# Optimization experiments

Hardware: AMD Instinct MI355X
Metric: run time of the kernel (lower is better)

## Reference

```python
import jax, jax.numpy as jnp
import numpy as np

N_NODES = 50000
N_EDGES = 800000
D_MODEL = 256
NUM_HEADS = 8
HEAD_DIM = D_MODEL // NUM_HEADS
D_FF = 2 * D_MODEL
NEG_SLOPE = 0.2
BN_EPS = 1e-5


def setup_inputs() -> dict:
    key = jax.random.key(0)
    ks = jax.random.split(key, 16)
    x = jax.random.normal(ks[0], (N_NODES, D_MODEL), dtype=jnp.float32)
    # edges guaranteed self-loop-free (remove_self_loops is then a no-op)
    src = jax.random.randint(ks[1], (N_EDGES,), 0, N_NODES)
    off = jax.random.randint(ks[2], (N_EDGES,), 1, N_NODES)
    dst = (src + off) % N_NODES
    edge_index = jnp.stack([src, dst]).astype(jnp.int64)

    def lin(k, fi, fo):
        s = 1.0 / np.sqrt(fi)
        return jax.random.uniform(k, (fi, fo), jnp.float32, -s, s)

    inp = {
        'x': x, 'edge_index': edge_index,
        'Wq': lin(ks[3], D_MODEL, D_MODEL), 'bq': jnp.zeros((D_MODEL,), jnp.float32),
        'Wk': lin(ks[4], D_MODEL, D_MODEL), 'bk': jnp.zeros((D_MODEL,), jnp.float32),
        'Wv': lin(ks[5], D_MODEL, D_MODEL), 'bv': jnp.zeros((D_MODEL,), jnp.float32),
        'Wo': lin(ks[6], D_MODEL, D_MODEL), 'bo': jnp.zeros((D_MODEL,), jnp.float32),
        'W1': lin(ks[7], D_MODEL, D_FF), 'b1': jnp.zeros((D_FF,), jnp.float32),
        'W2': lin(ks[8], D_FF, D_MODEL), 'b2': jnp.zeros((D_MODEL,), jnp.float32),
        'bn1_g': jnp.ones((D_MODEL,), jnp.float32), 'bn1_b': jnp.zeros((D_MODEL,), jnp.float32),
        'bn2_g': jnp.ones((D_MODEL,), jnp.float32), 'bn2_b': jnp.zeros((D_MODEL,), jnp.float32),
    }
    return inp


def _batch_norm(h, g, b):
    mean = jnp.mean(h, axis=0)
    var = jnp.mean((h - mean) ** 2, axis=0)  # biased var, torch BN training mode
    return (h - mean) * jax.lax.rsqrt(var + BN_EPS) * g + b


def reference(x, edge_index, Wq, bq, Wk, bk, Wv, bv, Wo, bo, W1, b1, W2, b2,
              bn1_g, bn1_b, bn2_g, bn2_b):
    N = x.shape[0]
    Qh = (x @ Wq + bq).reshape(N, NUM_HEADS, HEAD_DIM)
    Kh = (x @ Wk + bk).reshape(N, NUM_HEADS, HEAD_DIM)
    Vh = (x @ Wv + bv).reshape(N, NUM_HEADS, HEAD_DIM)
    # per-node score q_n . k_n / sqrt(C)  -> [N, H]
    s = jnp.einsum('nhc,nhc->nh', Qh, Kh) / jnp.sqrt(jnp.float32(HEAD_DIM))

    # add self loops (input edges contain no self loops)
    loops = jnp.arange(N, dtype=edge_index.dtype)
    src = jnp.concatenate([edge_index[0], loops])
    dst = jnp.concatenate([edge_index[1], loops])

    alpha = jax.nn.leaky_relu(s[src] + s[dst], NEG_SLOPE)  # [Etot, H]
    # segment softmax over destination neighborhoods
    m = jax.ops.segment_max(alpha, dst, num_segments=N)
    e = jnp.exp(alpha - m[dst])
    denom = jax.ops.segment_sum(e, dst, num_segments=N)
    a = e / denom[dst]

    msg = Vh[src] * a[:, :, None]                     # [Etot, H, C]
    attn = jax.ops.segment_sum(msg, dst, num_segments=N).reshape(N, D_MODEL)

    h = attn @ Wo + bo
    h = x + h
    h = _batch_norm(h, bn1_g, bn1_b)
    h2 = jax.nn.relu(h @ W1 + b1) @ W2 + b2
    h = _batch_norm(h + h2, bn2_g, bn2_b)
    return h
```

## Files before the change

### kernel.cpp

```cpp
#include <hip/hip_runtime.h>
#include <hip/hip_bf16.h>

#define NN 50000
#define MP 50048
#define DM 256
#define NH 8
#define HD 32
#define DFF 512

typedef unsigned short u16;
typedef unsigned char u8;
typedef __attribute__((ext_vector_type(8))) short bf16x8;
typedef __attribute__((ext_vector_type(4))) short bf16x4;
typedef __attribute__((ext_vector_type(4))) float f32x4;

__device__ __forceinline__ float leaky(float a) { return a > 0.f ? a : 0.2f * a; }

__device__ __forceinline__ float b2f(u16 s) {
    union { float f; unsigned u; } v; v.u = ((unsigned)s) << 16; return v.f;
}
__device__ __forceinline__ u16 f2b(float f) {
    union { float f; unsigned u; } v; v.f = f;
    unsigned r = v.u + 0x7FFFu + ((v.u >> 16) & 1u);
    return (u16)(r >> 16);
}

__device__ __forceinline__ void f8enc8(const float* v, unsigned* w2) {
#if __has_builtin(__builtin_amdgcn_cvt_pk_fp8_f32)
    int lo = 0, hi = 0;
    lo = __builtin_amdgcn_cvt_pk_fp8_f32(v[0], v[1], lo, false);
    lo = __builtin_amdgcn_cvt_pk_fp8_f32(v[2], v[3], lo, true);
    hi = __builtin_amdgcn_cvt_pk_fp8_f32(v[4], v[5], hi, false);
    hi = __builtin_amdgcn_cvt_pk_fp8_f32(v[6], v[7], hi, true);
    w2[0] = (unsigned)lo; w2[1] = (unsigned)hi;
#else
    unsigned r[8];
#pragma unroll
    for (int j = 0; j < 8; ++j) {
        union { float f; unsigned u; } x; x.f = v[j];
        const unsigned s = (x.u >> 24) & 0x80u;
        float a = fabsf(v[j]);
        if (a > 448.f) a = 448.f;
        if (a < 0.0009765625f) { r[j] = s; continue; }
        if (a < 0.015625f) {
            int m = (int)(a * 512.f + 0.5f); if (m > 7) m = 7;
            r[j] = s | (unsigned)m; continue;
        }
        union { float f; unsigned u; } w; w.f = a;
        unsigned rr = w.u + 0x7FFFFu + ((w.u >> 20) & 1u);
        int e2 = (int)((rr >> 23) & 0xffu) - 127;
        unsigned m3 = (rr >> 20) & 7u;
        if (e2 > 8) { e2 = 8; m3 = 7u; }
        r[j] = s | ((unsigned)(e2 + 7) << 3) | m3;
    }
    w2[0] = r[0] | (r[1] << 8) | (r[2] << 16) | (r[3] << 24);
    w2[1] = r[4] | (r[5] << 8) | (r[6] << 16) | (r[7] << 24);
#endif
}

__device__ __forceinline__ void f8dec8(uint2 uv, float* f) {
#if __has_builtin(__builtin_amdgcn_cvt_pk_f32_fp8)
    auto p0 = __builtin_amdgcn_cvt_pk_f32_fp8((int)uv.x, false);
    auto p1 = __builtin_amdgcn_cvt_pk_f32_fp8((int)uv.x, true);
    auto p2 = __builtin_amdgcn_cvt_pk_f32_fp8((int)uv.y, false);
    auto p3 = __builtin_amdgcn_cvt_pk_f32_fp8((int)uv.y, true);
    f[0] = p0[0]; f[1] = p0[1]; f[2] = p1[0]; f[3] = p1[1];
    f[4] = p2[0]; f[5] = p2[1]; f[6] = p3[0]; f[7] = p3[1];
#else
#pragma unroll
    for (int j = 0; j < 8; ++j) {
        const unsigned b = (j < 4 ? uv.x >> (8 * j) : uv.y >> (8 * (j - 4))) & 0xffu;
        const unsigned s = (b & 0x80u) << 24;
        const unsigned em = b & 0x7fu;
        union { unsigned u; float f; } n; n.u = s | ((em + 0x3C0u) << 20);
        float dn = (float)(int)(em & 7u) * 0.001953125f;
        dn = (b & 0x80u) ? -dn : dn;
        f[j] = (em >= 8u) ? n.f : dn;
    }
#endif
}

#define ASYNC16(gp, lp) __builtin_amdgcn_global_load_lds( \
    (const __attribute__((address_space(1))) void*)(gp),  \
    (__attribute__((address_space(3))) void*)(lp), 16, 0, 0)

template<int RELU, int RES, int K, int MODE>
__global__ __launch_bounds__(256, 4) void gemm_bf16(
    const u16* __restrict__ A, const u16* __restrict__ Bt,
    const float* __restrict__ bias, const void* __restrict__ res,
    const float* __restrict__ ra, const float* __restrict__ rb,
    u16* __restrict__ C, u8* __restrict__ Cv, float* __restrict__ gsums,
    int M, int N)
{
    union SMu {
        struct { u16 As[128][64]; u16 Bs[128][64]; } t;
        struct { u16 eps[128][136]; float lsum[128], lsq[128]; } e;
    };
    __shared__ __align__(16) SMu sm;

    const int tid = threadIdx.x;
    const int wave = tid >> 6, lane = tid & 63;

    const int gx = gridDim.x;
    const int nwg = gx * gridDim.y;
    const int orig = blockIdx.y * gx + blockIdx.x;
    const int q = nwg >> 3, r = nwg & 7;
    const int xcd = orig & 7, rank = orig >> 3;
    const int wg = (xcd < r ? xcd * (q + 1) : r * (q + 1) + (xcd - r) * q) + rank;
    const int m0 = (wg / gx) * 128, n0 = (wg % gx) * 128;

    const int wr = (wave >> 1) * 64, wc = (wave & 1) * 64;

    f32x4 acc[4][4] = {};

    const int srow = wave * 32 + (lane >> 3);
    const int scol = ((lane & 7) * 8) ^ (((lane >> 3) & 7) << 3);
    const int rx = (lane & 7) << 4;

#pragma unroll
    for (int k0 = 0; k0 < K; k0 += 64) {
#pragma unroll
        for (int i = 0; i < 4; ++i)
            ASYNC16(A + (size_t)(m0 + srow + i * 8) * K + k0 + scol,
                    &sm.t.As[wave * 32 + i * 8][0]);
#pragma unroll
        for (int i = 0; i < 4; ++i)
            ASYNC16(Bt + (size_t)(n0 + srow + i * 8) * K + k0 + scol,
                    &sm.t.Bs[wave * 32 + i * 8][0]);
        __syncthreads();
        const char* asb = (const char*)&sm.t.As[0][0];
        const char* bsb = (const char*)&sm.t.Bs[0][0];
#pragma unroll
        for (int kk = 0; kk < 64; kk += 32) {
            const int kb = (kk + (lane >> 4) * 8) * 2;
            bf16x8 av[4], bv[4];
#pragma unroll
            for (int m = 0; m < 4; ++m) {
                const int rr_ = wr + m * 16 + (lane & 15);
                av[m] = *(const bf16x8*)(asb + rr_ * 128 + (kb ^ rx));
            }
#pragma unroll
            for (int n = 0; n < 4; ++n) {
                const int rr_ = wc + n * 16 + (lane & 15);
                bv[n] = *(const bf16x8*)(bsb + rr_ * 128 + (kb ^ rx));
            }
#pragma unroll
            for (int m = 0; m < 4; ++m)
#pragma unroll
                for (int n = 0; n < 4; ++n)
                    acc[m][n] = __builtin_amdgcn_mfma_f32_16x16x32_bf16(
                        av[m], bv[n], acc[m][n], 0, 0, 0);
        }
        __syncthreads();
    }

    const int col_l = lane & 15, rgrp = (lane >> 4) * 4;
#pragma unroll
    for (int m = 0; m < 4; ++m)
#pragma unroll
        for (int rr2 = 0; rr2 < 4; ++rr2) {
            const int lr = wr + m * 16 + rgrp + rr2;
#pragma unroll
            for (int n = 0; n < 4; ++n)
                sm.e.eps[lr][wc + n * 16 + col_l] = f2b(acc[m][n][rr2]);
        }
    __syncthreads();
    if (MODE == 2) {
        if (tid < 128) { sm.e.lsum[tid] = 0.f; sm.e.lsq[tid] = 0.f; }
        __syncthreads();
    }

    const int tc = (tid & 15) * 8;
    float bb[8];
    *(float4*)(bb)     = *(const float4*)(bias + n0 + tc);
    *(float4*)(bb + 4) = *(const float4*)(bias + n0 + tc + 4);
    float ra8[8], rb8[8];
    if (RES == 3) {
        *(float4*)(ra8)     = *(const float4*)(ra + n0 + tc);
        *(float4*)(ra8 + 4) = *(const float4*)(ra + n0 + tc + 4);
        *(float4*)(rb8)     = *(const float4*)(rb + n0 + tc);
        *(float4*)(rb8 + 4) = *(const float4*)(rb + n0 + tc + 4);
    }
    float psum[8] = {}, psq[8] = {};
    const bool v8 = (MODE == 1) && (n0 >= 512);
    u16* dstb = (MODE == 1) ? C + n0 : C + n0;
    size_t dstride = (MODE == 1) ? 512 : (size_t)N;
    u8* vdst = v8 ? (Cv + (n0 - 512)) : nullptr;

#pragma unroll
    for (int it = 0; it < 8; ++it) {
        const int tr = (tid >> 4) + it * 16;
        const int row = m0 + tr;
        if (row < M) {
            bf16x8 cv = *(const bf16x8*)((const char*)&sm.e.eps[0][0] + tr * 272 + tc * 2);
            float v[8];
#pragma unroll
            for (int j = 0; j < 8; ++j) v[j] = b2f((u16)cv[j]) + bb[j];
            if (RES == 1) {
                const float* rp = (const float*)res + (size_t)row * N + n0 + tc;
                float4 r0 = *(const float4*)(rp);
                float4 r1 = *(const float4*)(rp + 4);
                v[0] += r0.x; v[1] += r0.y; v[2] += r0.z; v[3] += r0.w;
                v[4] += r1.x; v[5] += r1.y; v[6] += r1.z; v[7] += r1.w;
            }
            if (RES == 2) {
                bf16x8 rv = *(const bf16x8*)((const u16*)res + (size_t)row * N + n0 + tc);
#pragma unroll
                for (int j = 0; j < 8; ++j) v[j] += b2f((u16)rv[j]);
            }
            if (RES == 3) {
                bf16x8 rv = *(const bf16x8*)((const u16*)res + (size_t)row * N + n0 + tc);
#pragma unroll
                for (int j = 0; j < 8; ++j) v[j] += b2f((u16)rv[j]) * ra8[j] + rb8[j];
            }
            if (RELU) {
#pragma unroll
                for (int j = 0; j < 8; ++j) v[j] = fmaxf(v[j], 0.f);
            }
            if (MODE == 2) {
#pragma unroll
                for (int j = 0; j < 8; ++j) { psum[j] += v[j]; psq[j] += v[j] * v[j]; }
            }
            if (v8) {
                unsigned w2[2];
                f8enc8(v, w2);
                *(uint2*)(vdst + (size_t)row * 256 + tc) = make_uint2(w2[0], w2[1]);
            } else {
                u16 o[8];
#pragma unroll
                for (int j = 0; j < 8; ++j) o[j] = f2b(v[j]);
                *(bf16x8*)(dstb + (size_t)row * dstride + tc) = *(bf16x8*)o;
            }
        }
    }

    if (MODE == 2) {
#pragma unroll
        for (int j = 0; j < 8; ++j) {
            atomicAdd(&sm.e.lsum[tc + j], psum[j]);
            atomicAdd(&sm.e.lsq[tc + j], psq[j]);
        }
        __syncthreads();
        if (tid < 128) {
            atomicAdd(&gsums[n0 + tid], sm.e.lsum[tid]);
            atomicAdd(&gsums[DM + n0 + tid], sm.e.lsq[tid]);
        }
    }
}

__global__ __launch_bounds__(256) void prep_kernel(
    const float* __restrict__ x, u16* __restrict__ xb,
    const float* __restrict__ Wq, const float* __restrict__ Wk,
    const float* __restrict__ Wv, const float* __restrict__ Wo,
    const float* __restrict__ W1, const float* __restrict__ W2,
    u16* __restrict__ wqkvt, u16* __restrict__ wot,
    u16* __restrict__ w1t, u16* __restrict__ w2t,
    const float* __restrict__ bq, const float* __restrict__ bk,
    const float* __restrict__ bv, float* __restrict__ bqkv,
    const int* __restrict__ edst, int* __restrict__ counts, int E)
{
    const int b = blockIdx.x;
    if (b < 6250) {
        const size_t i = ((size_t)b * 256 + threadIdx.x) * 8;
        float4 a = *(const float4*)(x + i);
        float4 c = *(const float4*)(x + i + 4);
        u16 o[8] = {f2b(a.x), f2b(a.y), f2b(a.z), f2b(a.w),
                    f2b(c.x), f2b(c.y), f2b(c.z), f2b(c.w)};
        *(bf16x8*)(xb + i) = *(bf16x8*)o;
    } else if (b < 6378) {
        __shared__ float tile[64][65];
        const int tb = b - 6250;
        const float* Wsrc; u16* outp; int srcN, outS, n0, k0;
        if (tb < 64) {
            const int mi = tb >> 4, ti = tb & 15;
            n0 = (ti & 3) * 64; k0 = (ti >> 2) * 64;
            srcN = 256; outS = 256;
            if (mi == 0)      { Wsrc = Wq; outp = wqkvt; }
            else if (mi == 1) { Wsrc = Wk; outp = wqkvt + 256 * 256; }
            else if (mi == 2) { Wsrc = Wv; outp = wqkvt + 512 * 256; }
            else              { Wsrc = Wo; outp = wot; }
        } else if (tb < 96) {
            const int ti = tb - 64;
            n0 = (ti & 7) * 64; k0 = (ti >> 3) * 64;
            srcN = 512; outS = 256; Wsrc = W1; outp = w1t;
        } else {
            const int ti = tb - 96;
            n0 = (ti & 3) * 64; k0 = (ti >> 2) * 64;
            srcN = 256; outS = 512; Wsrc = W2; outp = w2t;
        }
        const int kr = threadIdx.x >> 4, cc = (threadIdx.x & 15) * 4;
#pragma unroll
        for (int j = 0; j < 4; ++j) {
            float4 v = *(const float4*)(Wsrc + (size_t)(k0 + kr + j * 16) * srcN + n0 + cc);
            tile[kr + j * 16][cc + 0] = v.x;
            tile[kr + j * 16][cc + 1] = v.y;
            tile[kr + j * 16][cc + 2] = v.z;
            tile[kr + j * 16][cc + 3] = v.w;
        }
        __syncthreads();
        const int nr = threadIdx.x >> 3, c2 = (threadIdx.x & 7) * 8;
#pragma unroll
        for (int p = 0; p < 2; ++p) {
            const int row = nr + p * 32;
            u16 o[8];
#pragma unroll
            for (int j = 0; j < 8; ++j) o[j] = f2b(tile[c2 + j][row]);
            *(bf16x8*)(outp + (size_t)(n0 + row) * outS + k0 + c2) = *(bf16x8*)o;
        }
    } else if (b == 6378) {
        const int t = threadIdx.x;
        bqkv[t] = bq[t]; bqkv[t + 256] = bk[t]; bqkv[t + 512] = bv[t];
    } else {
        const int e = (b - 6379) * 256 + threadIdx.x;
        if (e < E) atomicAdd(&counts[edst[e]], 1);
    }
}

__global__ __launch_bounds__(256) void bnfold_kernel(
    const float* __restrict__ sums, const float* __restrict__ g,
    const float* __restrict__ be, u16* __restrict__ w1t,
    const float* __restrict__ W1, const float* __restrict__ b1,
    float* __restrict__ b1p, float* __restrict__ affa, float* __restrict__ affc)
{
    const int blk = blockIdx.x;
    const int k = threadIdx.x;
    const float invM = 1.f / (float)NN;
    const float mean = sums[k] * invM;
    const float var = sums[DM + k] * invM - mean * mean;
    const float a = g[k] * rsqrtf(var + 1e-5f);
    const float c = be[k] - mean * a;
    if (blk < 64) {
#pragma unroll
        for (int j = 0; j < 8; ++j) {
            u16* pp = w1t + (size_t)(blk * 8 + j) * 256 + k;
            *pp = f2b(b2f(*pp) * a);
        }
    } else {
        __shared__ float cs[256];
        cs[k] = c;
        if (blk == 64) { affa[k] = a; affc[k] = c; }
        __syncthreads();
        const int n = (blk - 64) * 256 + k;
        float acc = b1[n];
        for (int kk = 0; kk < 256; ++kk)
            acc += cs[kk] * W1[(size_t)kk * 512 + n];
        b1p[n] = acc;
    }
}

__global__ __launch_bounds__(256) void scorefill_kernel(
    const u16* __restrict__ QK, float* __restrict__ s,
    const int* __restrict__ esrc, const int* __restrict__ edst,
    int* __restrict__ cursor, int* __restrict__ csr, int E, int nsb)
{
    const int b = blockIdx.x;
    if (b < nsb) {
        const int t = b * 256 + threadIdx.x;
        if (t >= NN * NH) return;
        const int n = t >> 3, h = t & 7;
        const u16* qp = QK + (size_t)n * 512 + h * HD;
        const u16* kp = qp + DM;
        float acc = 0.f;
#pragma unroll
        for (int c = 0; c < HD; c += 8) {
            bf16x8 qa = *(const bf16x8*)(qp + c);
            bf16x8 ka = *(const bf16x8*)(kp + c);
#pragma unroll
            for (int j = 0; j < 8; ++j)
                acc += b2f((u16)qa[j]) * b2f((u16)ka[j]);
        }
        s[t] = acc * 0.17677669529663687f;
    } else {
        const int e = (b - nsb) * 256 + threadIdx.x;
        if (e >= E) return;
        const int p = atomicAdd(&cursor[edst[e]], 1);
        csr[p] = esrc[e];
    }
}

__global__ __launch_bounds__(1024) void scan_kernel(
    const int* __restrict__ counts, int* __restrict__ offs,
    int* __restrict__ cursor, int n)
{
    __shared__ int wsum[16];
    __shared__ int srun;
    const int tid = threadIdx.x, lane = tid & 63, wid = tid >> 6;
    if (tid == 0) srun = 0;
    for (int base = 0; base < n; base += 4096) {
        const int idx = base + tid * 4;
        int v0 = 0, v1 = 0, v2 = 0, v3 = 0;
        if (idx + 3 < n) {
            int4 qv = *(const int4*)(counts + idx);
            v0 = qv.x; v1 = qv.y; v2 = qv.z; v3 = qv.w;
        } else if (idx < n) {
            v0 = counts[idx];
            if (idx + 1 < n) v1 = counts[idx + 1];
            if (idx + 2 < n) v2 = counts[idx + 2];
        }
        const int tsum = v0 + v1 + v2 + v3;
        int sc = tsum;
#pragma unroll
        for (int off = 1; off < 64; off <<= 1) {
            int t = __shfl_up(sc, off);
            if (lane >= off) sc += t;
        }
        if (lane == 63) wsum[wid] = sc;
        __syncthreads();
        if (tid < 16) {
            int w = wsum[tid];
#pragma unroll
            for (int off = 1; off < 16; off <<= 1) {
                int t = __shfl_up(w, off);
                if (tid >= off) w += t;
            }
            wsum[tid] = w;
        }
        __syncthreads();
        const int run = srun;
        int e = run + (wid ? wsum[wid - 1] : 0) + sc - tsum;
        if (idx < n)     { offs[idx] = e;     cursor[idx] = e; }
        e += v0;
        if (idx + 1 < n) { offs[idx + 1] = e; cursor[idx + 1] = e; }
        e += v1;
        if (idx + 2 < n) { offs[idx + 2] = e; cursor[idx + 2] = e; }
        e += v2;
        if (idx + 3 < n) { offs[idx + 3] = e; cursor[idx + 3] = e; }
        const int tot = wsum[15];
        __syncthreads();
        if (tid == 0) srun = run + tot;
    }
    if (tid == 0) offs[n] = srun;
}

__global__ __launch_bounds__(256) void aggregate_kernel(
    const float* __restrict__ s, const u8* __restrict__ V,
    const int* __restrict__ offs, const int* __restrict__ srcs,
    u16* __restrict__ attn)
{
    const int n = (blockIdx.x * 256 + threadIdx.x) >> 6;
    const int lane = threadIdx.x & 63;
    if (n >= NN) return;
    const int base = offs[n];
    const int deg = offs[n + 1] - base;
    const int half = lane >> 5;
    const int l = lane & 31;
    const int f0 = l * 8;
    const int h0 = l >> 2;
    const float snh = s[(size_t)n * 8 + h0];

    float a[8] = {};
    float d = 0.f;
    if (half == 0) {
        const float w = __expf(fminf(leaky(2.f * snh), 30.f));
        d = w;
        float vf[8];
        f8dec8(*(const uint2*)(V + (size_t)n * 256 + f0), vf);
#pragma unroll
        for (int j = 0; j < 8; ++j) a[j] = w * vf[j];
    }

    int i = 0;
    for (; i + 8 <= deg; i += 8) {
        const int sr0 = srcs[base + i + 0 + half];
        const int sr1 = srcs[base + i + 2 + half];
        const int sr2 = srcs[base + i + 4 + half];
        const int sr3 = srcs[base + i + 6 + half];
        const float sv0 = s[(size_t)sr0 * 8 + h0];
        const float sv1 = s[(size_t)sr1 * 8 + h0];
        const float sv2 = s[(size_t)sr2 * 8 + h0];
        const float sv3 = s[(size_t)sr3 * 8 + h0];
        uint2 q0 = *(const uint2*)(V + (size_t)sr0 * 256 + f0);
        uint2 q1 = *(const uint2*)(V + (size_t)sr1 * 256 + f0);
        uint2 q2 = *(const uint2*)(V + (size_t)sr2 * 256 + f0);
        uint2 q3 = *(const uint2*)(V + (size_t)sr3 * 256 + f0);
        const float w0 = __expf(fminf(leaky(snh + sv0), 30.f));
        const float w1 = __expf(fminf(leaky(snh + sv1), 30.f));
        const float w2 = __expf(fminf(leaky(snh + sv2), 30.f));
        const float w3 = __expf(fminf(leaky(snh + sv3), 30.f));
        d += w0 + w1 + w2 + w3;
        float u0[8], u1[8], u2[8], u3[8];
        f8dec8(q0, u0); f8dec8(q1, u1); f8dec8(q2, u2); f8dec8(q3, u3);
#pragma unroll
        for (int j = 0; j < 8; ++j)
            a[j] += w0 * u0[j] + w1 * u1[j] + w2 * u2[j] + w3 * u3[j];
    }
    for (; i + 2 <= deg; i += 2) {
        const int sr = srcs[base + i + half];
        const float sv = s[(size_t)sr * 8 + h0];
        uint2 qv = *(const uint2*)(V + (size_t)sr * 256 + f0);
        const float w = __expf(fminf(leaky(snh + sv), 30.f));
        float uf[8];
        f8dec8(qv, uf);
        d += w;
#pragma unroll
        for (int j = 0; j < 8; ++j) a[j] += w * uf[j];
    }
    if (i < deg && half == 0) {
        const int sr = srcs[base + i];
        const float sv = s[(size_t)sr * 8 + h0];
        uint2 qv = *(const uint2*)(V + (size_t)sr * 256 + f0);
        const float w = __expf(fminf(leaky(snh + sv), 30.f));
        float uf[8];
        f8dec8(qv, uf);
        d += w;
#pragma unroll
        for (int j = 0; j < 8; ++j) a[j] += w * uf[j];
    }

    d += __shfl_xor(d, 32);
#pragma unroll
    for (int j = 0; j < 8; ++j) a[j] += __shfl_xor(a[j], 32);

    if (half == 0) {
        const float rd = 1.f / d;
        u16 o[8];
#pragma unroll
        for (int j = 0; j < 8; ++j) o[j] = f2b(a[j] * rd);
        *(bf16x8*)(attn + (size_t)n * DM + f0) = *(bf16x8*)o;
    }
}

__global__ __launch_bounds__(256) void apply_out_kernel(
    const u16* __restrict__ z, const float* __restrict__ sums,
    const float* __restrict__ g, const float* __restrict__ b,
    float* __restrict__ out)
{
    const size_t i = ((size_t)blockIdx.x * 256 + threadIdx.x) * 8;
    if (i >= (size_t)NN * DM) return;
    const int f0 = (int)(i & (DM - 1));
    const float invM = 1.f / (float)NN;
    bf16x8 v = *(const bf16x8*)(z + i);
    float o[8];
#pragma unroll
    for (int j = 0; j < 8; ++j) {
        const int f = f0 + j;
        const float mean = sums[f] * invM;
        const float var = sums[DM + f] * invM - mean * mean;
        const float a = g[f] * rsqrtf(var + 1e-5f);
        o[j] = b2f((u16)v[j]) * a + (b[f] - mean * a);
    }
    *(float4*)(out + i)     = *(float4*)(o);
    *(float4*)(out + i + 4) = *(float4*)(o + 4);
}

extern "C" void kernel_launch(void* const* d_in, const int* in_sizes, int n_in,
                              void* d_out, int out_size, void* d_ws, size_t ws_size,
                              hipStream_t stream)
{
    const float* x   = (const float*)d_in[0];
    const int* eidx  = (const int*)d_in[1];
    const int E      = in_sizes[1] / 2;
    const int* esrc  = eidx;
    const int* edst  = eidx + E;
    const float* Wq = (const float*)d_in[2];  const float* bq = (const float*)d_in[3];
    const float* Wk = (const float*)d_in[4];  const float* bk = (const float*)d_in[5];
    const float* Wv = (const float*)d_in[6];  const float* bv = (const float*)d_in[7];
    const float* Wo = (const float*)d_in[8];  const float* bo = (const float*)d_in[9];
    const float* W1 = (const float*)d_in[10]; const float* b1 = (const float*)d_in[11];
    const float* W2 = (const float*)d_in[12]; const float* b2 = (const float*)d_in[13];
    const float* g1 = (const float*)d_in[14]; const float* be1 = (const float*)d_in[15];
    const float* g2 = (const float*)d_in[16]; const float* be2 = (const float*)d_in[17];
    float* out = (float*)d_out;

    u16* xb  = (u16*)d_ws;
    u16* qk  = xb + (size_t)MP * DM;
    u8*  vb  = (u8*)(qk + (size_t)MP * 512);
    u16* attn = (u16*)(vb) + (size_t)MP * DM;
    float* sS = (float*)(attn + (size_t)MP * DM);
    int* counts = (int*)(sS + (size_t)NN * NH);
    int* offs   = counts + NN;
    int* cursor = offs + NN + 1;
    int* csr    = cursor + NN;
    uintptr_t p = (uintptr_t)(csr + E);
    p = (p + 15) & ~(uintptr_t)15;
    u16* wqkvt = (u16*)p;
    u16* wot   = wqkvt + 768 * 256;
    u16* w1t   = wot + 256 * 256;
    u16* w2t   = w1t + 512 * 256;
    float* bqkv   = (float*)(w2t + 256 * 512);
    float* bnsum1 = bqkv + 768;
    float* bnsum2 = bnsum1 + 512;
    float* b1p    = bnsum2 + 512;
    float* affa   = b1p + 512;
    float* affc   = affa + 256;

    const dim3 blk(256);
    const int elem_grid = (NN * DM / 8 + 255) / 256;
    const int hist_blks = (E + 255) / 256;
    const int nsb = (NN * NH + 255) / 256;

    hipMemsetAsync(counts, 0, sizeof(int) * NN, stream);
    hipMemsetAsync(bnsum1, 0, sizeof(float) * 1024, stream);
    prep_kernel<<<6379 + hist_blks, blk, 0, stream>>>(
        x, xb, Wq, Wk, Wv, Wo, W1, W2, wqkvt, wot, w1t, w2t,
        bq, bk, bv, bqkv, edst, counts, E);
    scan_kernel<<<1, 1024, 0, stream>>>(counts, offs, cursor, NN);

    gemm_bf16<0, 0, 256, 1><<<dim3(6, MP / 128), blk, 0, stream>>>(
        xb, wqkvt, bqkv, nullptr, nullptr, nullptr, qk, vb, nullptr, NN, 768);

    scorefill_kernel<<<nsb + hist_blks, blk, 0, stream>>>(
        qk, sS, esrc, edst, cursor, csr, E, nsb);

    aggregate_kernel<<<(NN + 3) / 4, blk, 0, stream>>>(sS, vb, offs, csr, attn);

    gemm_bf16<0, 2, 256, 2><<<dim3(2, MP / 128), blk, 0, stream>>>(
        attn, wot, bo, xb, nullptr, nullptr, xb, nullptr, bnsum1, NN, DM);

    bnfold_kernel<<<66, blk, 0, stream>>>(bnsum1, g1, be1, w1t, W1, b1,
                                          b1p, affa, affc);

    gemm_bf16<1, 0, 256, 0><<<dim3(4, MP / 128), blk, 0, stream>>>(
        xb, w1t, b1p, nullptr, nullptr, nullptr, qk, nullptr, nullptr, NN, DFF);

    gemm_bf16<0, 3, 512, 2><<<dim3(2, MP / 128), blk, 0, stream>>>(
        qk, w2t, b2, xb, affa, affc, attn, nullptr, bnsum2, NN, DM);

    apply_out_kernel<<<elem_grid, blk, 0, stream>>>(attn, bnsum2, g2, be2, out);
}
```

Measured before the change: 358.7 us.

## Halve GEMM epilogue LDS staging and vectorize edge histogram/CSR fill

The GEMM epilogue now stages the output tile through LDS in two 64-row halves instead of one 128-row buffer. This shrinks the epilogue part of the shared-memory union, though the As/Bs tiles still set its overall size. The edge-count histogram and CSR scatter each handle four edges per thread with int4 loads, and the CSR writes use nontemporal stores. The GEMM grids use 391 row tiles (MROWS) instead of MP/128, which is also 391, so the launch shape does not change. The split epilogue adds barriers, and the vectorized edge loads assume 16-byte alignment of the edge arrays.

```diff
diff --git a/kernel.cpp b/kernel.cpp
--- a/kernel.cpp
+++ b/kernel.cpp
@@ -3,6 +3,7 @@
 
 #define NN 50000
 #define MP 50048
+#define MROWS 391
 #define DM 256
 #define NH 8
 #define HD 32
@@ -94,7 +95,7 @@
 {
     union SMu {
         struct { u16 As[128][64]; u16 Bs[128][64]; } t;
-        struct { u16 eps[128][136]; float lsum[128], lsq[128]; } e;
+        struct { u16 eps[64][136]; float lsum[128], lsq[128]; } e;
     };
     __shared__ __align__(16) SMu sm;
 
@@ -155,22 +156,10 @@
     }
 
     const int col_l = lane & 15, rgrp = (lane >> 4) * 4;
-#pragma unroll
-    for (int m = 0; m < 4; ++m)
-#pragma unroll
-        for (int rr2 = 0; rr2 < 4; ++rr2) {
-            const int lr = wr + m * 16 + rgrp + rr2;
-#pragma unroll
-            for (int n = 0; n < 4; ++n)
-                sm.e.eps[lr][wc + n * 16 + col_l] = f2b(acc[m][n][rr2]);
-        }
-    __syncthreads();
-    if (MODE == 2) {
-        if (tid < 128) { sm.e.lsum[tid] = 0.f; sm.e.lsq[tid] = 0.f; }
-        __syncthreads();
-    }
-
     const int tc = (tid & 15) * 8;
+
+    if (MODE == 2 && tid < 128) { sm.e.lsum[tid] = 0.f; sm.e.lsq[tid] = 0.f; }
+
     float bb[8];
     *(float4*)(bb)     = *(const float4*)(bias + n0 + tc);
     *(float4*)(bb + 4) = *(const float4*)(bias + n0 + tc + 4);
@@ -183,58 +172,79 @@
     }
     float psum[8] = {}, psq[8] = {};
     const bool v8 = (MODE == 1) && (n0 >= 512);
-    u16* dstb = (MODE == 1) ? C + n0 : C + n0;
+    u16* dstb = C + n0;
     size_t dstride = (MODE == 1) ? 512 : (size_t)N;
     u8* vdst = v8 ? (Cv + (n0 - 512)) : nullptr;
 
 #pragma unroll
-    for (int it = 0; it < 8; ++it) {
-        const int tr = (tid >> 4) + it * 16;
-        const int row = m0 + tr;
-        if (row < M) {
-            bf16x8 cv = *(const bf16x8*)((const char*)&sm.e.eps[0][0] + tr * 272 + tc * 2);
-            float v[8];
-#pragma unroll
-            for (int j = 0; j < 8; ++j) v[j] = b2f((u16)cv[j]) + bb[j];
-            if (RES == 1) {
-                const float* rp = (const float*)res + (size_t)row * N + n0 + tc;
-                float4 r0 = *(const float4*)(rp);
-                float4 r1 = *(const float4*)(rp + 4);
-                v[0] += r0.x; v[1] += r0.y; v[2] += r0.z; v[3] += r0.w;
-                v[4] += r1.x; v[5] += r1.y; v[6] += r1.z; v[7] += r1.w;
+    for (int hf = 0; hf < 2; ++hf) {
+        if (hf) __syncthreads();
+        if ((wave >> 1) == hf) {
+#pragma unroll
+            for (int m = 0; m < 4; ++m)
+#pragma unroll
+                for (int rr2 = 0; rr2 < 4; ++rr2) {
+                    const int lr = m * 16 + rgrp + rr2;
+#pragma unroll
+                    for (int n = 0; n < 4; ++n)
+                        sm.e.eps[lr][wc + n * 16 + col_l] = f2b(acc[m][n][rr2]);
+                }
+        }
+        __syncthreads();
+#pragma unroll
+        for (int it = 0; it < 4; ++it) {
+            const int tr = (tid >> 4) + it * 16;
+            const int row = m0 + hf * 64 + tr;
+            if (row < M) {
+                bf16x8 cv = *(const bf16x8*)((const char*)&sm.e.eps[0][0]
+                                             + tr * 272 + tc * 2);
+                float v[8];
+#pragma unroll
+                for (int j = 0; j < 8; ++j) v[j] = b2f((u16)cv[j]) + bb[j];
+                if (RES == 1) {
+                    const float* rp = (const float*)res + (size_t)row * N + n0 + tc;
+                    float4 r0 = *(const float4*)(rp);
+                    float4 r1 = *(const float4*)(rp + 4);
+                    v[0] += r0.x; v[1] += r0.y; v[2] += r0.z; v[3] += r0.w;
+                    v[4] += r1.x; v[5] += r1.y; v[6] += r1.z; v[7] += r1.w;
+                }
+                if (RES == 2) {
+                    bf16x8 rv = *(const bf16x8*)((const u16*)res
+                                                 + (size_t)row * N + n0 + tc);
+#pragma unroll
+                    for (int j = 0; j < 8; ++j) v[j] += b2f((u16)rv[j]);
+                }
+                if (RES == 3) {
+                    bf16x8 rv = *(const bf16x8*)((const u16*)res
+                                                 + (size_t)row * N + n0 + tc);
+#pragma unroll
+                    for (int j = 0; j < 8; ++j)
+                        v[j] += b2f((u16)rv[j]) * ra8[j] + rb8[j];
+                }
+                if (RELU) {
+#pragma unroll
+                    for (int j = 0; j < 8; ++j) v[j] = fmaxf(v[j], 0.f);
+                }
+                if (MODE == 2) {
+#pragma unroll
+                    for (int j = 0; j < 8; ++j) { psum[j] += v[j]; psq[j] += v[j] * v[j]; }
+                }
+                if (v8) {
+                    unsigned w2[2];
+                    f8enc8(v, w2);
+                    *(uint2*)(vdst + (size_t)row * 256 + tc) = make_uint2(w2[0], w2[1]);
+                } else {
+                    u16 o[8];
+#pragma unroll
+                    for (int j = 0; j < 8; ++j) o[j] = f2b(v[j]);
+                    *(bf16x8*)(dstb + (size_t)row * dstride + tc) = *(bf16x8*)o;
+                }
             }
-            if (RES == 2) {
-                bf16x8 rv = *(const bf16x8*)((const u16*)res + (size_t)row * N + n0 + tc);
-#pragma unroll
-                for (int j = 0; j < 8; ++j) v[j] += b2f((u16)rv[j]);
-            }
-            if (RES == 3) {
-                bf16x8 rv = *(const bf16x8*)((const u16*)res + (size_t)row * N + n0 + tc);
-#pragma unroll
-                for (int j = 0; j < 8; ++j) v[j] += b2f((u16)rv[j]) * ra8[j] + rb8[j];
-            }
-            if (RELU) {
-#pragma unroll
-                for (int j = 0; j < 8; ++j) v[j] = fmaxf(v[j], 0.f);
-            }
-            if (MODE == 2) {
-#pragma unroll
-                for (int j = 0; j < 8; ++j) { psum[j] += v[j]; psq[j] += v[j] * v[j]; }
-            }
-            if (v8) {
-                unsigned w2[2];
-                f8enc8(v, w2);
-                *(uint2*)(vdst + (size_t)row * 256 + tc) = make_uint2(w2[0], w2[1]);
-            } else {
-                u16 o[8];
-#pragma unroll
-                for (int j = 0; j < 8; ++j) o[j] = f2b(v[j]);
-                *(bf16x8*)(dstb + (size_t)row * dstride + tc) = *(bf16x8*)o;
-            }
         }
     }
 
     if (MODE == 2) {
+        __syncthreads();
 #pragma unroll
         for (int j = 0; j < 8; ++j) {
             atomicAdd(&sm.e.lsum[tc + j], psum[j]);
@@ -311,8 +321,16 @@
         const int t = threadIdx.x;
         bqkv[t] = bq[t]; bqkv[t + 256] = bk[t]; bqkv[t + 512] = bv[t];
     } else {
-        const int e = (b - 6379) * 256 + threadIdx.x;
-        if (e < E) atomicAdd(&counts[edst[e]], 1);
+        const int e0 = ((b - 6379) * 256 + (int)threadIdx.x) * 4;
+        if (e0 + 3 < E) {
+            const int4 d4 = *(const int4*)(edst + e0);
+            atomicAdd(&counts[d4.x], 1);
+            atomicAdd(&counts[d4.y], 1);
+            atomicAdd(&counts[d4.z], 1);
+            atomicAdd(&counts[d4.w], 1);
+        } else {
+            for (int e = e0; e < E; ++e) atomicAdd(&counts[edst[e]], 1);
+        }
     }
 }
 
@@ -371,10 +389,24 @@
         }
         s[t] = acc * 0.17677669529663687f;
     } else {
-        const int e = (b - nsb) * 256 + threadIdx.x;
-        if (e >= E) return;
-        const int p = atomicAdd(&cursor[edst[e]], 1);
-        csr[p] = esrc[e];
+        const int e0 = ((b - nsb) * 256 + (int)threadIdx.x) * 4;
+        if (e0 + 3 < E) {
+            const int4 s4 = *(const int4*)(esrc + e0);
+            const int4 d4 = *(const int4*)(edst + e0);
+            const int p0 = atomicAdd(&cursor[d4.x], 1);
+            const int p1 = atomicAdd(&cursor[d4.y], 1);
+            const int p2 = atomicAdd(&cursor[d4.z], 1);
+            const int p3 = atomicAdd(&cursor[d4.w], 1);
+            __builtin_nontemporal_store(s4.x, &csr[p0]);
+            __builtin_nontemporal_store(s4.y, &csr[p1]);
+            __builtin_nontemporal_store(s4.z, &csr[p2]);
+            __builtin_nontemporal_store(s4.w, &csr[p3]);
+        } else {
+            for (int e = e0; e < E; ++e) {
+                const int p = atomicAdd(&cursor[edst[e]], 1);
+                csr[p] = esrc[e];
+            }
+        }
     }
 }
 
@@ -586,7 +618,7 @@
 
     const dim3 blk(256);
     const int elem_grid = (NN * DM / 8 + 255) / 256;
-    const int hist_blks = (E + 255) / 256;
+    const int hist_blks = (E / 4 + 255) / 256;
     const int nsb = (NN * NH + 255) / 256;
 
     hipMemsetAsync(counts, 0, sizeof(int) * NN, stream);
@@ -596,7 +628,7 @@
         bq, bk, bv, bqkv, edst, counts, E);
     scan_kernel<<<1, 1024, 0, stream>>>(counts, offs, cursor, NN);
 
-    gemm_bf16<0, 0, 256, 1><<<dim3(6, MP / 128), blk, 0, stream>>>(
+    gemm_bf16<0, 0, 256, 1><<<dim3(6, MROWS), blk, 0, stream>>>(
         xb, wqkvt, bqkv, nullptr, nullptr, nullptr, qk, vb, nullptr, NN, 768);
 
     scorefill_kernel<<<nsb + hist_blks, blk, 0, stream>>>(
@@ -604,16 +636,16 @@
 
     aggregate_kernel<<<(NN + 3) / 4, blk, 0, stream>>>(sS, vb, offs, csr, attn);
 
-    gemm_bf16<0, 2, 256, 2><<<dim3(2, MP / 128), blk, 0, stream>>>(
+    gemm_bf16<0, 2, 256, 2><<<dim3(2, MROWS), blk, 0, stream>>>(
         attn, wot, bo, xb, nullptr, nullptr, xb, nullptr, bnsum1, NN, DM);
 
     bnfold_kernel<<<66, blk, 0, stream>>>(bnsum1, g1, be1, w1t, W1, b1,
                                           b1p, affa, affc);
 
-    gemm_bf16<1, 0, 256, 0><<<dim3(4, MP / 128), blk, 0, stream>>>(
+    gemm_bf16<1, 0, 256, 0><<<dim3(4, MROWS), blk, 0, stream>>>(
         xb, w1t, b1p, nullptr, nullptr, nullptr, qk, nullptr, nullptr, NN, DFF);
 
-    gemm_bf16<0, 3, 512, 2><<<dim3(2, MP / 128), blk, 0, stream>>>(
+    gemm_bf16<0, 3, 512, 2><<<dim3(2, MROWS), blk, 0, stream>>>(
         qk, w2t, b2, xb, affa, affc, attn, nullptr, bnsum2, NN, DM);
 
     apply_out_kernel<<<elem_grid, blk, 0, stream>>>(attn, bnsum2, g2, be2, out);
```

Result: slower. 411.2 us (+14.6%).
